# Performance work log

Hardware: AMD Instinct MI355X
Metric: run time of the kernel (lower is better)

The kernel has to match this reference:

```python
import jax, jax.numpy as jnp
import numpy as np

NUM_COLUMNS = 16
INPUT_DIM = 1024
NUM_NEURONS = 256
SPARSITY = 0.05
B, S = 4, 2048


def setup_inputs() -> dict:
    key = jax.random.key(0)
    ks = jax.random.split(key, 12)
    D, C, N = INPUT_DIM, NUM_COLUMNS, NUM_NEURONS
    inp = {
        'x': jax.random.normal(ks[0], (B, S, D), dtype=jnp.float32),
        'col_emb': jax.random.normal(ks[1], (C, D), dtype=jnp.float32) * 0.02,
        'gate_w1': jax.random.normal(ks[2], (D, D // 2), dtype=jnp.float32) / np.sqrt(D),
        'gate_b1': jnp.zeros((D // 2,), dtype=jnp.float32),
        'gate_w2': jax.random.normal(ks[3], (D // 2, C), dtype=jnp.float32) / np.sqrt(D // 2),
        'gate_b2': jnp.zeros((C,), dtype=jnp.float32),
        'W_cols': jax.random.normal(ks[4], (C, D, N), dtype=jnp.float32) / np.sqrt(D),
        'b_cols': jnp.zeros((C, N), dtype=jnp.float32),
        'proj_w': jax.random.normal(ks[5], (C * N, D), dtype=jnp.float32) / np.sqrt(C * N),
        'proj_b': jnp.zeros((D,), dtype=jnp.float32),
        'ln_g': jnp.ones((D,), dtype=jnp.float32),
        'ln_b': jnp.zeros((D,), dtype=jnp.float32),
    }
    return inp


def _l2norm(v, axis=-1, eps=1e-12):
    n = jnp.sqrt(jnp.sum(v * v, axis=axis, keepdims=True))
    return v / jnp.maximum(n, eps)


def reference(x, col_emb, gate_w1, gate_b1, gate_w2, gate_b2, W_cols, b_cols,
              proj_w, proj_b, ln_g, ln_b):
    Bq, Sq, D = x.shape
    C = col_emb.shape[0]
    # --- router ---
    similarity = jnp.einsum('bsd,cd->bsc', _l2norm(x), _l2norm(col_emb))
    h = jax.nn.gelu(x @ gate_w1 + gate_b1, approximate=False)
    gate_values = jax.nn.sigmoid(h @ gate_w2 + gate_b2)
    logits = similarity + gate_values  # [B,S,C]
    k = max(1, int(C * SPARSITY))
    _, top_idx = jax.lax.top_k(logits, k)
    mask = jnp.sum(jax.nn.one_hot(top_idx, C, dtype=logits.dtype), axis=-2)  # [B,S,C]
    weights = mask * jax.nn.softmax(logits, axis=-1)
    # --- per-column compute (grouped GEMM), weighted combine ---
    cols = jax.nn.gelu(jnp.einsum('bsd,cdn->bscn', x, W_cols) + b_cols,
                       approximate=False)  # [B,S,C,N]
    cols = cols * weights[..., None]
    combined = cols.reshape(Bq, Sq, -1)  # [B,S,C*N], column-major concat order
    # --- proj + residual + layernorm ---
    y = combined @ proj_w + proj_b + x
    mu = jnp.mean(y, axis=-1, keepdims=True)
    var = jnp.mean((y - mu) ** 2, axis=-1, keepdims=True)
    out = (y - mu) * jax.lax.rsqrt(var + 1e-5) * ln_g + ln_b
    return out
```

## Files before the change

### kernel.cpp

```cpp
#include <hip/hip_runtime.h>
#include <hip/hip_bf16.h>
#include <math.h>

#define D    1024
#define C    16
#define N    256
#define TOK  8192
#define DH   512
#define RT_T 16
#define WLG  160
#define BCAP 20

using bf16x8 = __attribute__((ext_vector_type(8))) short;
using f32x4  = __attribute__((ext_vector_type(4))) float;

__device__ __forceinline__ float gelu_exact(float v) {
    return 0.5f * v * (1.0f + erff(v * 0.70710678118654752440f));
}
__device__ __forceinline__ float sigmoidf_(float z) {
    return 1.0f / (1.0f + expf(-z));
}
__device__ __forceinline__ short f2bf(float f) {
    unsigned u = __float_as_uint(f);
    unsigned r = u + 0x7FFF + ((u >> 16) & 1);
    return (short)(r >> 16);
}
__device__ __forceinline__ float bf2f(short s) {
    return __uint_as_float(((unsigned)(unsigned short)s) << 16);
}

__device__ __forceinline__ void tconv_body(const float* __restrict__ src0,
        short* __restrict__ dst0, int R, int Cc, int bx, int by, int bz,
        float (*tile)[65], int tid) {
    const size_t bofs = (size_t)bz * R * Cc;
    const float* src = src0 + bofs;
    short* dst = dst0 + bofs;
    const int cBase = bx * 64;
    const int rBase = by * 64;
    const int rr = tid >> 4;
    const int cq = (tid & 15) * 4;
    #pragma unroll
    for (int h = 0; h < 4; ++h) {
        const int r = h * 16 + rr;
        const float4 v = *(const float4*)&src[(size_t)(rBase + r) * Cc + cBase + cq];
        tile[r][cq + 0] = v.x; tile[r][cq + 1] = v.y;
        tile[r][cq + 2] = v.z; tile[r][cq + 3] = v.w;
    }
    __syncthreads();
    #pragma unroll
    for (int h = 0; h < 4; ++h) {
        const int cc = h * 16 + rr;
        short4 o;
        o.x = f2bf(tile[cq + 0][cc]);
        o.y = f2bf(tile[cq + 1][cc]);
        o.z = f2bf(tile[cq + 2][cc]);
        o.w = f2bf(tile[cq + 3][cc]);
        *(short4*)&dst[(size_t)(cBase + cc) * R + rBase + cq] = o;
    }
}

__global__ __launch_bounds__(256) void prep_all_kernel(
        const float* __restrict__ x, const float* __restrict__ col_emb,
        const float* __restrict__ gate_w1, const float* __restrict__ W_cols,
        const float* __restrict__ proj_w,
        short* __restrict__ xb, short* __restrict__ w1T,
        short* __restrict__ WcT, short* __restrict__ pwT,
        float* __restrict__ cnorm) {
    __shared__ float tile[64][65];
    const int b = blockIdx.x;
    const int tid = threadIdx.x;
    if (b == 0) {
        const int c = tid >> 4, l = tid & 15;
        float acc = 0.f;
        for (int j = 0; j < 64; ++j) {
            float v = col_emb[c * D + l + 16 * j];
            acc += v * v;
        }
        for (int off = 8; off; off >>= 1) acc += __shfl_xor(acc, off, 16);
        if (l == 0) cnorm[c] = fmaxf(sqrtf(acc), 1e-12f);
    } else if (b < 2049) {
        const int base = (b - 1) * 1024;
        #pragma unroll
        for (int h = 0; h < 4; ++h) {
            const int i = base + h * 256 + tid;
            const float4 v = ((const float4*)x)[i];
            short4 o;
            o.x = f2bf(v.x); o.y = f2bf(v.y); o.z = f2bf(v.z); o.w = f2bf(v.w);
            ((short4*)xb)[i] = o;
        }
    } else if (b < 2177) {
        const int idx = b - 2049;
        tconv_body(gate_w1, w1T, D, DH, idx & 7, idx >> 3, 0, tile, tid);
    } else if (b < 3201) {
        const int idx = b - 2177;
        tconv_body(W_cols, WcT, D, N, idx & 3, (idx >> 2) & 15, idx >> 6, tile, tid);
    } else {
        const int idx = b - 3201;
        tconv_body(proj_w, pwT, N, D, idx & 15, (idx >> 4) & 3, idx >> 6, tile, tid);
    }
}

__global__ __launch_bounds__(256) void gate_mfma_kernel(
        const short* __restrict__ Ag, const short* __restrict__ BTg,
        const float* __restrict__ bias, short* __restrict__ outb) {
    __shared__ short As[128 * 64];
    __shared__ short Bs[64 * 64];
    const int tid = threadIdx.x;
    const int lane = tid & 63;
    const int wave = tid >> 6;
    const int wr = wave >> 1, wc = wave & 1;

    const int rS = tid >> 3;
    const int bo = (tid & 7) * 16;
    const size_t m0 = (size_t)blockIdx.x * 128;
    const int n0 = blockIdx.y * 64;

    const char* gA = (const char*)Ag + (m0 + rS) * (D * 2) + bo;
    const char* gB = (const char*)BTg + ((size_t)(n0 + rS)) * (D * 2) + bo;

    const int mrow = lane & 15;
    const int kb0 = (lane >> 4) * 16;

    f32x4 acc[4][2] = {};
    for (int kk = 0; kk < D / 64; ++kk) {
        #pragma unroll
        for (int h = 0; h < 4; ++h) {
            const int r = rS + 32 * h;
            *(bf16x8*)((char*)As + r * 128 + (bo ^ ((r & 7) << 4))) =
                *(const bf16x8*)(gA + (size_t)(32 * h) * (D * 2));
        }
        #pragma unroll
        for (int h = 0; h < 2; ++h) {
            const int r = rS + 32 * h;
            *(bf16x8*)((char*)Bs + r * 128 + (bo ^ ((r & 7) << 4))) =
                *(const bf16x8*)(gB + (size_t)(32 * h) * (D * 2));
        }
        gA += 128; gB += 128;
        __syncthreads();
        #pragma unroll
        for (int ks = 0; ks < 2; ++ks) {
            const int kb = kb0 + ks * 64;
            bf16x8 aF[4], bF[2];
            #pragma unroll
            for (int i = 0; i < 4; ++i) {
                const int m = wr * 64 + i * 16 + mrow;
                aF[i] = *(const bf16x8*)((const char*)As + m * 128 + (kb ^ ((m & 7) << 4)));
            }
            #pragma unroll
            for (int j = 0; j < 2; ++j) {
                const int n = wc * 32 + j * 16 + mrow;
                bF[j] = *(const bf16x8*)((const char*)Bs + n * 128 + (kb ^ ((n & 7) << 4)));
            }
            #pragma unroll
            for (int i = 0; i < 4; ++i)
                #pragma unroll
                for (int j = 0; j < 2; ++j)
                    acc[i][j] = __builtin_amdgcn_mfma_f32_16x16x32_bf16(
                                    aF[i], bF[j], acc[i][j], 0, 0, 0);
        }
        __syncthreads();
    }
    const int crow = (lane >> 4) * 4;
    const int ccol = lane & 15;
    #pragma unroll
    for (int i = 0; i < 4; ++i)
        #pragma unroll
        for (int j = 0; j < 2; ++j) {
            const int n = n0 + wc * 32 + j * 16 + ccol;
            const float bb = bias[n];
            #pragma unroll
            for (int r = 0; r < 4; ++r) {
                const int m = (int)m0 + wr * 64 + i * 16 + crow + r;
                outb[(size_t)m * DH + n] = f2bf(gelu_exact(acc[i][j][r] + bb));
            }
        }
}

template<int MODE>
__global__ __launch_bounds__(256) void mfma_tile(
        const short* __restrict__ Ag, const short* __restrict__ BTg,
        const float* __restrict__ bias, const float* __restrict__ x,
        const int* __restrict__ order, const float* __restrict__ wgt,
        const int* __restrict__ wl,
        short* __restrict__ outb, float* __restrict__ outf) {
    constexpr int KDIM = (MODE == 2) ? N : D;
    constexpr int KSTEPS = KDIM / 64;
    __shared__ short As[64 * 64];
    __shared__ short Bs[128 * 64];
    __shared__ int   tokl[64];
    __shared__ float wgl[64];

    const int e = wl[blockIdx.x];
    if (e < 0) return;
    const int col  = e >> 24;
    const int nt   = (e >> 16) & 0xFF;
    const int base = e & 0xFFFF;

    const int tid = threadIdx.x;
    const int lane = tid & 63;
    const int wave = tid >> 6;
    const int wr = wave >> 1, wc = wave & 1;
    const int n0 = blockIdx.y * 128;

    if (tid < 64) {
        const int i = tid < nt ? tid : nt - 1;
        const int t = order[base + i];
        tokl[tid] = t;
        if (MODE == 1) wgl[tid] = wgt[t];
    }
    __syncthreads();

    const int rS = tid >> 3;
    const int bo = (tid & 7) * 16;
    const char* gA0; const char* gA1;
    if (MODE == 1) {
        gA0 = (const char*)Ag + (size_t)tokl[rS] * (D * 2) + bo;
        gA1 = (const char*)Ag + (size_t)tokl[rS + 32] * (D * 2) + bo;
    } else {
        const int s0 = base + min(rS, nt - 1);
        const int s1 = base + min(rS + 32, nt - 1);
        gA0 = (const char*)Ag + (size_t)s0 * (N * 2) + bo;
        gA1 = (const char*)Ag + (size_t)s1 * (N * 2) + bo;
    }
    const size_t bRowB = KDIM * 2;
    size_t bbase;
    if (MODE == 1) bbase = ((size_t)col * N + n0) * bRowB;
    else           bbase = ((size_t)col * D + n0) * bRowB;
    const char* gB = (const char*)BTg + bbase + (size_t)rS * bRowB + bo;

    const int mrow = lane & 15;
    const int kb0 = (lane >> 4) * 16;

    f32x4 acc[2][4] = {};
    for (int kk = 0; kk < KSTEPS; ++kk) {
        {
            const int r0 = rS, r1 = rS + 32;
            *(bf16x8*)((char*)As + r0 * 128 + (bo ^ ((r0 & 7) << 4))) = *(const bf16x8*)gA0;
            *(bf16x8*)((char*)As + r1 * 128 + (bo ^ ((r1 & 7) << 4))) = *(const bf16x8*)gA1;
        }
        #pragma unroll
        for (int h = 0; h < 4; ++h) {
            const int r = rS + 32 * h;
            *(bf16x8*)((char*)Bs + r * 128 + (bo ^ ((r & 7) << 4))) =
                *(const bf16x8*)(gB + (size_t)(32 * h) * bRowB);
        }
        gA0 += 128; gA1 += 128; gB += 128;
        __syncthreads();
        #pragma unroll
        for (int ks = 0; ks < 2; ++ks) {
            const int kb = kb0 + ks * 64;
            bf16x8 aF[2], bF[4];
            #pragma unroll
            for (int i = 0; i < 2; ++i) {
                const int m = wr * 32 + i * 16 + mrow;
                aF[i] = *(const bf16x8*)((const char*)As + m * 128 + (kb ^ ((m & 7) << 4)));
            }
            #pragma unroll
            for (int j = 0; j < 4; ++j) {
                const int n = wc * 64 + j * 16 + mrow;
                bF[j] = *(const bf16x8*)((const char*)Bs + n * 128 + (kb ^ ((n & 7) << 4)));
            }
            #pragma unroll
            for (int i = 0; i < 2; ++i)
                #pragma unroll
                for (int j = 0; j < 4; ++j)
                    acc[i][j] = __builtin_amdgcn_mfma_f32_16x16x32_bf16(
                                    aF[i], bF[j], acc[i][j], 0, 0, 0);
        }
        __syncthreads();
    }

    const int crow = (lane >> 4) * 4;
    const int ccol = lane & 15;
    if (MODE == 1) {
        #pragma unroll
        for (int i = 0; i < 2; ++i)
            #pragma unroll
            for (int j = 0; j < 4; ++j) {
                const int n = n0 + wc * 64 + j * 16 + ccol;
                const float bb = bias[col * N + n];
                #pragma unroll
                for (int r = 0; r < 4; ++r) {
                    const int il = wr * 32 + i * 16 + crow + r;
                    if (il < nt) {
                        const float v = gelu_exact(acc[i][j][r] + bb) * wgl[il];
                        outb[(size_t)(base + il) * N + n] = f2bf(v);
                    }
                }
            }
    } else {
        #pragma unroll
        for (int i = 0; i < 2; ++i)
            #pragma unroll
            for (int j = 0; j < 4; ++j) {
                const int dcol = n0 + wc * 64 + j * 16 + ccol;
                const float bb = bias[dcol];
                #pragma unroll
                for (int r = 0; r < 4; ++r) {
                    const int il = wr * 32 + i * 16 + crow + r;
                    if (il < nt) {
                        const size_t ofs = (size_t)tokl[il] * D + dcol;
                        outf[ofs] = acc[i][j][r] + bb + x[ofs];
                    }
                }
            }
    }
}

__global__ __launch_bounds__(256) void route_kernel(
        const float* __restrict__ x, const short* __restrict__ Hb,
        const float* __restrict__ col_emb, const float* __restrict__ cnorm,
        const float* __restrict__ w2, const float* __restrict__ b2,
        int* __restrict__ idx, float* __restrict__ wgt) {
    __shared__ float P[256][33];
    __shared__ float Q[8][33];
    __shared__ float SSW[4];
    __shared__ float FL[RT_T][34];
    const int tid = threadIdx.x;
    const int lane = tid & 63;
    const int t0 = blockIdx.x * RT_T;
    const int swz = (tid & 7) << 2;

    float4 ce[C];
    #pragma unroll
    for (int c = 0; c < C; ++c)
        ce[c] = *(const float4*)&col_emb[c * D + tid * 4];
    float w2r[2][C];
    #pragma unroll
    for (int r2 = 0; r2 < 2; ++r2)
        #pragma unroll
        for (int cq = 0; cq < 4; ++cq) {
            const float4 v = *(const float4*)&w2[(tid * 2 + r2) * C + cq * 4];
            w2r[r2][cq * 4 + 0] = v.x; w2r[r2][cq * 4 + 1] = v.y;
            w2r[r2][cq * 4 + 2] = v.z; w2r[r2][cq * 4 + 3] = v.w;
        }

    for (int ti = 0; ti < RT_T; ++ti) {
        const int t = t0 + ti;
        const float4 xv = *(const float4*)&x[(size_t)t * D + tid * 4];
        const unsigned hu = *(const unsigned*)&Hb[(size_t)t * DH + tid * 2];
        const float h0 = bf2f((short)(hu & 0xffff));
        const float h1 = bf2f((short)(hu >> 16));
        float pv[32];
        #pragma unroll
        for (int c = 0; c < C; ++c)
            pv[c] = xv.x * ce[c].x + xv.y * ce[c].y + xv.z * ce[c].z + xv.w * ce[c].w;
        #pragma unroll
        for (int c = 0; c < C; ++c)
            pv[C + c] = h0 * w2r[0][c] + h1 * w2r[1][c];
        float ssp = xv.x * xv.x + xv.y * xv.y + xv.z * xv.z + xv.w * xv.w;
        #pragma unroll
        for (int off = 32; off; off >>= 1) ssp += __shfl_xor(ssp, off);
        if (lane == 0) SSW[tid >> 6] = ssp;
        #pragma unroll
        for (int c = 0; c < 32; ++c)
            P[tid][c ^ swz] = pv[c];
        __syncthreads();
        {
            const int v = tid & 31, jj = tid >> 5;
            float s = 0.f;
            #pragma unroll
            for (int k = 0; k < 32; ++k) {
                const int row = jj * 32 + k;
                s += P[row][v ^ ((row & 7) << 2)];
            }
            Q[jj][v] = s;
        }
        __syncthreads();
        if (tid < 32) {
            float f = 0.f;
            #pragma unroll
            for (int j2 = 0; j2 < 8; ++j2) f += Q[j2][tid];
            FL[ti][tid] = f;
        } else if (tid == 32) {
            FL[ti][32] = SSW[0] + SSW[1] + SSW[2] + SSW[3];
        }
        __syncthreads();
    }

    if (tid < RT_T) {
        const int t = t0 + tid;
        const float xn = fmaxf(sqrtf(FL[tid][32]), 1e-12f);
        float logit[C];
        #pragma unroll
        for (int c = 0; c < C; ++c)
            logit[c] = FL[tid][c] / (xn * cnorm[c])
                     + sigmoidf_(FL[tid][C + c] + b2[c]);
        float mx = logit[0]; int am = 0;
        #pragma unroll
        for (int c = 1; c < C; ++c)
            if (logit[c] > mx) { mx = logit[c]; am = c; }
        float se = 0.f;
        #pragma unroll
        for (int c = 0; c < C; ++c) se += expf(logit[c] - mx);
        idx[t] = am;
        wgt[t] = 1.f / se;
    }
}

__global__ __launch_bounds__(256) void hist_kernel(const int* __restrict__ idx,
        int* __restrict__ cursor, int* __restrict__ wl) {
    __shared__ int h[C];
    const int tid = threadIdx.x;
    if (tid < C) h[tid] = 0;
    for (int i = tid; i < WLG; i += 256) wl[i] = -1;
    __syncthreads();
    for (int t = tid; t < TOK; t += 256) atomicAdd(&h[idx[t]], 1);
    __syncthreads();
    if (tid == 0) {
        int s = 0;
        int slots[8] = {0, 0, 0, 0, 0, 0, 0, 0};
        for (int c = 0; c < C; ++c) {
            cursor[c] = s;
            for (int st = 0; st < h[c]; st += 64) {
                const int ntg = min(64, h[c] - st);
                int b = c & 7;
                while (slots[b] >= BCAP) b = (b + 1) & 7;
                wl[slots[b] * 8 + b] = (c << 24) | (ntg << 16) | (s + st);
                slots[b]++;
            }
            s += h[c];
        }
    }
}

__global__ __launch_bounds__(256) void scatter_kernel(const int* __restrict__ idx,
        int* __restrict__ cursor, int* __restrict__ order) {
    __shared__ int lh[C];
    __shared__ int lbase[C];
    const int tid = threadIdx.x;
    const int t = blockIdx.x * 256 + tid;
    if (tid < C) lh[tid] = 0;
    __syncthreads();
    const int c = idx[t];
    const int p = atomicAdd(&lh[c], 1);
    __syncthreads();
    if (tid < C) lbase[tid] = atomicAdd(&cursor[tid], lh[tid]);
    __syncthreads();
    order[lbase[c] + p] = t;
}

__global__ __launch_bounds__(256) void ln_kernel(float* __restrict__ out,
        const float* __restrict__ g, const float* __restrict__ b) {
    __shared__ float wr_[4], wr2[4];
    const int t = blockIdx.x, tid = threadIdx.x;
    const float4 v = *(const float4*)&out[(size_t)t * D + tid * 4];
    float s = v.x + v.y + v.z + v.w;
    float s2 = v.x * v.x + v.y * v.y + v.z * v.z + v.w * v.w;
    for (int off = 32; off; off >>= 1) { s += __shfl_xor(s, off); s2 += __shfl_xor(s2, off); }
    if ((tid & 63) == 0) { wr_[tid >> 6] = s; wr2[tid >> 6] = s2; }
    __syncthreads();
    const float sum = wr_[0] + wr_[1] + wr_[2] + wr_[3];
    const float sum2 = wr2[0] + wr2[1] + wr2[2] + wr2[3];
    const float mu = sum * (1.f / D);
    const float var = sum2 * (1.f / D) - mu * mu;
    const float inv = rsqrtf(var + 1e-5f);
    const float4 g4 = *(const float4*)&g[tid * 4];
    const float4 b4 = *(const float4*)&b[tid * 4];
    float4 o;
    o.x = (v.x - mu) * inv * g4.x + b4.x;
    o.y = (v.y - mu) * inv * g4.y + b4.y;
    o.z = (v.z - mu) * inv * g4.z + b4.z;
    o.w = (v.w - mu) * inv * g4.w + b4.w;
    *(float4*)&out[(size_t)t * D + tid * 4] = o;
}

extern "C" void kernel_launch(void* const* d_in, const int* in_sizes, int n_in,
                              void* d_out, int out_size, void* d_ws, size_t ws_size,
                              hipStream_t stream) {
    const float* x       = (const float*)d_in[0];
    const float* col_emb = (const float*)d_in[1];
    const float* gate_w1 = (const float*)d_in[2];
    const float* gate_b1 = (const float*)d_in[3];
    const float* gate_w2 = (const float*)d_in[4];
    const float* gate_b2 = (const float*)d_in[5];
    const float* W_cols  = (const float*)d_in[6];
    const float* b_cols  = (const float*)d_in[7];
    const float* proj_w  = (const float*)d_in[8];
    const float* proj_b  = (const float*)d_in[9];
    const float* ln_g    = (const float*)d_in[10];
    const float* ln_b    = (const float*)d_in[11];
    float* out = (float*)d_out;

    char* w = (char*)d_ws;
    short* xb    = (short*)w;  w += (size_t)TOK * D * 2;
    short* Hb    = (short*)w;  w += (size_t)TOK * DH * 2;
    short* actb  = (short*)w;  w += (size_t)TOK * N * 2 + 65536;
    short* w1T   = (short*)w;  w += (size_t)DH * D * 2;
    short* WcT   = (short*)w;  w += (size_t)C * N * D * 2;
    short* pwT   = (short*)w;  w += (size_t)C * D * N * 2;
    float* wgt   = (float*)w;  w += TOK * 4;
    float* cnorm = (float*)w;  w += 64;
    int*   idx   = (int*)w;    w += TOK * 4;
    int*   order = (int*)w;    w += TOK * 4;
    int*   cursor= (int*)w;    w += 64;
    int*   wl    = (int*)w;    w += WLG * 4;

    hipLaunchKernelGGL(prep_all_kernel, dim3(4225), dim3(256), 0, stream,
                       x, col_emb, gate_w1, W_cols, proj_w,
                       xb, w1T, WcT, pwT, cnorm);
    hipLaunchKernelGGL(gate_mfma_kernel, dim3(TOK / 128, DH / 64), dim3(256), 0, stream,
                       xb, w1T, gate_b1, Hb);
    hipLaunchKernelGGL(route_kernel, dim3(TOK / RT_T), dim3(256), 0, stream,
                       x, Hb, col_emb, cnorm, gate_w2, gate_b2, idx, wgt);
    hipLaunchKernelGGL(hist_kernel, dim3(1), dim3(256), 0, stream, idx, cursor, wl);
    hipLaunchKernelGGL(scatter_kernel, dim3(TOK / 256), dim3(256), 0, stream,
                       idx, cursor, order);
    hipLaunchKernelGGL((mfma_tile<1>), dim3(WLG, N / 128), dim3(256), 0, stream,
                       xb, WcT, b_cols, nullptr, order, wgt, wl, actb, nullptr);
    hipLaunchKernelGGL((mfma_tile<2>), dim3(WLG, D / 128), dim3(256), 0, stream,
                       actb, pwT, proj_b, x, order, wgt, wl, nullptr, out);
    hipLaunchKernelGGL(ln_kernel, dim3(TOK), dim3(256), 0, stream, out, ln_g, ln_b);
}
```

Before: 175.0 us.

## Double-buffer GEMM tiles via direct global-to-LDS loads with 64x64 tiles

The gate GEMM and both grouped expert GEMMs now stage A and B tiles into two LDS buffers using global_load_lds (direct global-to-LDS DMA). The next K-slice is prefetched while the current one feeds the MFMAs. Tiles shrink to 64x64 per block, which doubles grid size for more parallelism but lowers per-block data reuse. The pre-swizzled global addresses keep the XOR LDS layout, and the loop keeps one barrier per step.

```diff
diff --git a/kernel.cpp b/kernel.cpp
--- a/kernel.cpp
+++ b/kernel.cpp
@@ -28,6 +28,22 @@
 __device__ __forceinline__ float bf2f(short s) {
     return __uint_as_float(((unsigned)(unsigned short)s) << 16);
 }
+
+__device__ __forceinline__ void gload16(const void* g, void* l) {
+    __builtin_amdgcn_global_load_lds(
+        (const __attribute__((address_space(1))) unsigned int*)g,
+        (__attribute__((address_space(3))) unsigned int*)l, 16, 0, 0);
+}
+
+#define STAGE2(buf, kk) do {                                   \
+    const int ko_ = (kk) * 128;                                \
+    char* lA_ = (char*)AB[buf][0] + ldsWo;                     \
+    char* lB_ = (char*)AB[buf][1] + ldsWo;                     \
+    gload16(gA0 + ko_, lA_);                                   \
+    gload16(gA1 + ko_, lA_ + 1024);                            \
+    gload16(gB0 + ko_, lB_);                                   \
+    gload16(gB1 + ko_, lB_ + 1024);                            \
+} while (0)
 
 __device__ __forceinline__ void tconv_body(const float* __restrict__ src0,
         short* __restrict__ dst0, int R, int Cc, int bx, int by, int bz,
@@ -103,56 +119,52 @@
 __global__ __launch_bounds__(256) void gate_mfma_kernel(
         const short* __restrict__ Ag, const short* __restrict__ BTg,
         const float* __restrict__ bias, short* __restrict__ outb) {
-    __shared__ short As[128 * 64];
-    __shared__ short Bs[64 * 64];
+    __shared__ short AB[2][2][64 * 64];
     const int tid = threadIdx.x;
     const int lane = tid & 63;
     const int wave = tid >> 6;
     const int wr = wave >> 1, wc = wave & 1;
 
-    const int rS = tid >> 3;
-    const int bo = (tid & 7) * 16;
-    const size_t m0 = (size_t)blockIdx.x * 128;
+    const size_t m0 = (size_t)blockIdx.x * 64;
     const int n0 = blockIdx.y * 64;
 
-    const char* gA = (const char*)Ag + (m0 + rS) * (D * 2) + bo;
-    const char* gB = (const char*)BTg + ((size_t)(n0 + rS)) * (D * 2) + bo;
-
-    const int mrow = lane & 15;
+    const int r0 = wave * 16 + (lane >> 3);
+    const int r1 = r0 + 8;
+    const int bl = (lane & 7) * 16;
+    const int b0 = bl ^ ((r0 & 7) << 4);
+    const int b1 = bl ^ ((r1 & 7) << 4);
+    const char* gA0 = (const char*)Ag + (m0 + r0) * (size_t)(D * 2) + b0;
+    const char* gA1 = (const char*)Ag + (m0 + r1) * (size_t)(D * 2) + b1;
+    const char* gB0 = (const char*)BTg + (size_t)(n0 + r0) * (D * 2) + b0;
+    const char* gB1 = (const char*)BTg + (size_t)(n0 + r1) * (D * 2) + b1;
+    const int ldsWo = wave * 2048;
+
+    const int mrow = wr * 32 + (lane & 15);
+    const int nrow = wc * 32 + (lane & 15);
     const int kb0 = (lane >> 4) * 16;
-
-    f32x4 acc[4][2] = {};
+    const int swm = (mrow & 7) << 4;
+    const int swn = (nrow & 7) << 4;
+
+    f32x4 acc[2][2] = {};
+    STAGE2(0, 0);
+    __syncthreads();
     for (int kk = 0; kk < D / 64; ++kk) {
-        #pragma unroll
-        for (int h = 0; h < 4; ++h) {
-            const int r = rS + 32 * h;
-            *(bf16x8*)((char*)As + r * 128 + (bo ^ ((r & 7) << 4))) =
-                *(const bf16x8*)(gA + (size_t)(32 * h) * (D * 2));
-        }
-        #pragma unroll
-        for (int h = 0; h < 2; ++h) {
-            const int r = rS + 32 * h;
-            *(bf16x8*)((char*)Bs + r * 128 + (bo ^ ((r & 7) << 4))) =
-                *(const bf16x8*)(gB + (size_t)(32 * h) * (D * 2));
-        }
-        gA += 128; gB += 128;
-        __syncthreads();
+        const int cur = kk & 1;
+        if (kk + 1 < D / 64) STAGE2(cur ^ 1, kk + 1);
+        const char* As = (const char*)AB[cur][0];
+        const char* Bs = (const char*)AB[cur][1];
         #pragma unroll
         for (int ks = 0; ks < 2; ++ks) {
             const int kb = kb0 + ks * 64;
-            bf16x8 aF[4], bF[2];
-            #pragma unroll
-            for (int i = 0; i < 4; ++i) {
-                const int m = wr * 64 + i * 16 + mrow;
-                aF[i] = *(const bf16x8*)((const char*)As + m * 128 + (kb ^ ((m & 7) << 4)));
-            }
-            #pragma unroll
-            for (int j = 0; j < 2; ++j) {
-                const int n = wc * 32 + j * 16 + mrow;
-                bF[j] = *(const bf16x8*)((const char*)Bs + n * 128 + (kb ^ ((n & 7) << 4)));
-            }
-            #pragma unroll
-            for (int i = 0; i < 4; ++i)
+            bf16x8 aF[2], bF[2];
+            #pragma unroll
+            for (int i = 0; i < 2; ++i)
+                aF[i] = *(const bf16x8*)(As + (mrow + i * 16) * 128 + (kb ^ swm));
+            #pragma unroll
+            for (int j = 0; j < 2; ++j)
+                bF[j] = *(const bf16x8*)(Bs + (nrow + j * 16) * 128 + (kb ^ swn));
+            #pragma unroll
+            for (int i = 0; i < 2; ++i)
                 #pragma unroll
                 for (int j = 0; j < 2; ++j)
                     acc[i][j] = __builtin_amdgcn_mfma_f32_16x16x32_bf16(
@@ -163,14 +175,14 @@
     const int crow = (lane >> 4) * 4;
     const int ccol = lane & 15;
     #pragma unroll
-    for (int i = 0; i < 4; ++i)
+    for (int i = 0; i < 2; ++i)
         #pragma unroll
         for (int j = 0; j < 2; ++j) {
             const int n = n0 + wc * 32 + j * 16 + ccol;
             const float bb = bias[n];
             #pragma unroll
             for (int r = 0; r < 4; ++r) {
-                const int m = (int)m0 + wr * 64 + i * 16 + crow + r;
+                const int m = (int)m0 + wr * 32 + i * 16 + crow + r;
                 outb[(size_t)m * DH + n] = f2bf(gelu_exact(acc[i][j][r] + bb));
             }
         }
@@ -185,8 +197,7 @@
         short* __restrict__ outb, float* __restrict__ outf) {
     constexpr int KDIM = (MODE == 2) ? N : D;
     constexpr int KSTEPS = KDIM / 64;
-    __shared__ short As[64 * 64];
-    __shared__ short Bs[128 * 64];
+    __shared__ short AB[2][2][64 * 64];
     __shared__ int   tokl[64];
     __shared__ float wgl[64];
 
@@ -200,7 +211,7 @@
     const int lane = tid & 63;
     const int wave = tid >> 6;
     const int wr = wave >> 1, wc = wave & 1;
-    const int n0 = blockIdx.y * 128;
+    const int n0 = blockIdx.y * 64;
 
     if (tid < 64) {
         const int i = tid < nt ? tid : nt - 1;
@@ -210,60 +221,57 @@
     }
     __syncthreads();
 
-    const int rS = tid >> 3;
-    const int bo = (tid & 7) * 16;
+    const int r0 = wave * 16 + (lane >> 3);
+    const int r1 = r0 + 8;
+    const int bl = (lane & 7) * 16;
+    const int b0 = bl ^ ((r0 & 7) << 4);
+    const int b1 = bl ^ ((r1 & 7) << 4);
     const char* gA0; const char* gA1;
     if (MODE == 1) {
-        gA0 = (const char*)Ag + (size_t)tokl[rS] * (D * 2) + bo;
-        gA1 = (const char*)Ag + (size_t)tokl[rS + 32] * (D * 2) + bo;
+        gA0 = (const char*)Ag + (size_t)tokl[r0] * (D * 2) + b0;
+        gA1 = (const char*)Ag + (size_t)tokl[r1] * (D * 2) + b1;
     } else {
-        const int s0 = base + min(rS, nt - 1);
-        const int s1 = base + min(rS + 32, nt - 1);
-        gA0 = (const char*)Ag + (size_t)s0 * (N * 2) + bo;
-        gA1 = (const char*)Ag + (size_t)s1 * (N * 2) + bo;
+        const int s0 = base + min(r0, nt - 1);
+        const int s1 = base + min(r1, nt - 1);
+        gA0 = (const char*)Ag + (size_t)s0 * (N * 2) + b0;
+        gA1 = (const char*)Ag + (size_t)s1 * (N * 2) + b1;
     }
     const size_t bRowB = KDIM * 2;
     size_t bbase;
     if (MODE == 1) bbase = ((size_t)col * N + n0) * bRowB;
     else           bbase = ((size_t)col * D + n0) * bRowB;
-    const char* gB = (const char*)BTg + bbase + (size_t)rS * bRowB + bo;
-
-    const int mrow = lane & 15;
+    const char* gB0 = (const char*)BTg + bbase + (size_t)r0 * bRowB + b0;
+    const char* gB1 = (const char*)BTg + bbase + (size_t)r1 * bRowB + b1;
+    const int ldsWo = wave * 2048;
+
+    const int mrow = wr * 32 + (lane & 15);
+    const int nrow = wc * 32 + (lane & 15);
     const int kb0 = (lane >> 4) * 16;
-
-    f32x4 acc[2][4] = {};
+    const int swm = (mrow & 7) << 4;
+    const int swn = (nrow & 7) << 4;
+
+    f32x4 acc[2][2] = {};
+    STAGE2(0, 0);
+    __syncthreads();
     for (int kk = 0; kk < KSTEPS; ++kk) {
-        {
-            const int r0 = rS, r1 = rS + 32;
-            *(bf16x8*)((char*)As + r0 * 128 + (bo ^ ((r0 & 7) << 4))) = *(const bf16x8*)gA0;
-            *(bf16x8*)((char*)As + r1 * 128 + (bo ^ ((r1 & 7) << 4))) = *(const bf16x8*)gA1;
-        }
-        #pragma unroll
-        for (int h = 0; h < 4; ++h) {
-            const int r = rS + 32 * h;
-            *(bf16x8*)((char*)Bs + r * 128 + (bo ^ ((r & 7) << 4))) =
-                *(const bf16x8*)(gB + (size_t)(32 * h) * bRowB);
-        }
-        gA0 += 128; gA1 += 128; gB += 128;
-        __syncthreads();
+        const int cur = kk & 1;
+        if (kk + 1 < KSTEPS) STAGE2(cur ^ 1, kk + 1);
+        const char* As = (const char*)AB[cur][0];
+        const char* Bs = (const char*)AB[cur][1];
         #pragma unroll
         for (int ks = 0; ks < 2; ++ks) {
             const int kb = kb0 + ks * 64;
-            bf16x8 aF[2], bF[4];
-            #pragma unroll
-            for (int i = 0; i < 2; ++i) {
-                const int m = wr * 32 + i * 16 + mrow;
-                aF[i] = *(const bf16x8*)((const char*)As + m * 128 + (kb ^ ((m & 7) << 4)));
-            }
-            #pragma unroll
-            for (int j = 0; j < 4; ++j) {
-                const int n = wc * 64 + j * 16 + mrow;
-                bF[j] = *(const bf16x8*)((const char*)Bs + n * 128 + (kb ^ ((n & 7) << 4)));
-            }
+            bf16x8 aF[2], bF[2];
+            #pragma unroll
+            for (int i = 0; i < 2; ++i)
+                aF[i] = *(const bf16x8*)(As + (mrow + i * 16) * 128 + (kb ^ swm));
+            #pragma unroll
+            for (int j = 0; j < 2; ++j)
+                bF[j] = *(const bf16x8*)(Bs + (nrow + j * 16) * 128 + (kb ^ swn));
             #pragma unroll
             for (int i = 0; i < 2; ++i)
                 #pragma unroll
-                for (int j = 0; j < 4; ++j)
+                for (int j = 0; j < 2; ++j)
                     acc[i][j] = __builtin_amdgcn_mfma_f32_16x16x32_bf16(
                                     aF[i], bF[j], acc[i][j], 0, 0, 0);
         }
@@ -276,8 +284,8 @@
         #pragma unroll
         for (int i = 0; i < 2; ++i)
             #pragma unroll
-            for (int j = 0; j < 4; ++j) {
-                const int n = n0 + wc * 64 + j * 16 + ccol;
+            for (int j = 0; j < 2; ++j) {
+                const int n = n0 + wc * 32 + j * 16 + ccol;
                 const float bb = bias[col * N + n];
                 #pragma unroll
                 for (int r = 0; r < 4; ++r) {
@@ -292,8 +300,8 @@
         #pragma unroll
         for (int i = 0; i < 2; ++i)
             #pragma unroll
-            for (int j = 0; j < 4; ++j) {
-                const int dcol = n0 + wc * 64 + j * 16 + ccol;
+            for (int j = 0; j < 2; ++j) {
+                const int dcol = n0 + wc * 32 + j * 16 + ccol;
                 const float bb = bias[dcol];
                 #pragma unroll
                 for (int r = 0; r < 4; ++r) {
@@ -499,16 +507,16 @@
     hipLaunchKernelGGL(prep_all_kernel, dim3(4225), dim3(256), 0, stream,
                        x, col_emb, gate_w1, W_cols, proj_w,
                        xb, w1T, WcT, pwT, cnorm);
-    hipLaunchKernelGGL(gate_mfma_kernel, dim3(TOK / 128, DH / 64), dim3(256), 0, stream,
+    hipLaunchKernelGGL(gate_mfma_kernel, dim3(TOK / 64, DH / 64), dim3(256), 0, stream,
                        xb, w1T, gate_b1, Hb);
     hipLaunchKernelGGL(route_kernel, dim3(TOK / RT_T), dim3(256), 0, stream,
                        x, Hb, col_emb, cnorm, gate_w2, gate_b2, idx, wgt);
     hipLaunchKernelGGL(hist_kernel, dim3(1), dim3(256), 0, stream, idx, cursor, wl);
     hipLaunchKernelGGL(scatter_kernel, dim3(TOK / 256), dim3(256), 0, stream,
                        idx, cursor, order);
-    hipLaunchKernelGGL((mfma_tile<1>), dim3(WLG, N / 128), dim3(256), 0, stream,
+    hipLaunchKernelGGL((mfma_tile<1>), dim3(WLG, N / 64), dim3(256), 0, stream,
                        xb, WcT, b_cols, nullptr, order, wgt, wl, actb, nullptr);
-    hipLaunchKernelGGL((mfma_tile<2>), dim3(WLG, D / 128), dim3(256), 0, stream,
+    hipLaunchKernelGGL((mfma_tile<2>), dim3(WLG, D / 64), dim3(256), 0, stream,
                        actb, pwT, proj_b, x, order, wgt, wl, nullptr, out);
     hipLaunchKernelGGL(ln_kernel, dim3(TOK), dim3(256), 0, stream, out, ln_g, ln_b);
 }
```

After: 156.9 us. -10.3%, faster.
